# Optimization experiments

Measured on AMD Instinct MI355X. Metric: run time of the kernel, lower is better.

The kernel has to match this reference:

```python
import jax, jax.numpy as jnp
import numpy as np

N_NODES = 200000
N_EDGES = 3200000
N_FEAT = 128
N_GRAPHS = 1000
N_CLASSES = 10
K = 30          # sort-pool k
C_CAT = 97      # 32+32+32+1 concatenated channels


def _glorot(k, shape):
    fan = shape[0] + shape[-1]
    return jax.random.normal(k, shape, jnp.float32) * (2.0 / fan) ** 0.5


def setup_inputs() -> dict:
    key = jax.random.key(0)
    ks = jax.random.split(key, 20)
    x = jax.random.normal(ks[0], (N_NODES, N_FEAT), jnp.float32)
    edge_index = jax.random.randint(ks[1], (2, N_EDGES), 0, N_NODES, jnp.int32)
    batch = jnp.sort(jax.random.randint(ks[2], (N_NODES,), 0, N_GRAPHS, jnp.int32))
    params = dict(
        W1=_glorot(ks[3], (N_FEAT, 32)), b1=jnp.zeros((32,), jnp.float32),
        W2=_glorot(ks[4], (32, 32)),     b2=jnp.zeros((32,), jnp.float32),
        W3=_glorot(ks[5], (32, 32)),     b3=jnp.zeros((32,), jnp.float32),
        W4=_glorot(ks[6], (32, 1)),      b4=jnp.zeros((1,), jnp.float32),
        conv5_w=_glorot(ks[7], (16, 1, 97)),  conv5_b=jnp.zeros((16,), jnp.float32),
        conv6_w=_glorot(ks[8], (32, 16, 5)),  conv6_b=jnp.zeros((32,), jnp.float32),
        fc1_w=_glorot(ks[9], (352, 128)),     fc1_b=jnp.zeros((128,), jnp.float32),
        fc2_w=_glorot(ks[10], (128, N_CLASSES)), fc2_b=jnp.zeros((N_CLASSES,), jnp.float32),
    )
    return dict(x=x, edge_index=edge_index, batch=batch, **params)


def reference(x, edge_index, batch, W1, b1, W2, b2, W3, b3, W4, b4,
              conv5_w, conv5_b, conv6_w, conv6_b, fc1_w, fc1_b, fc2_w, fc2_b):
    N = x.shape[0]
    src, dst = edge_index[0], edge_index[1]
    emask = (src != dst).astype(x.dtype)            # remove_self_loops
    deg = jax.ops.segment_sum(emask, dst, num_segments=N) + 1.0  # +1 for added self-loop
    inv_sqrt = jax.lax.rsqrt(deg)
    coef = emask * inv_sqrt[src] * inv_sqrt[dst]    # D^-1/2 (A) D^-1/2 edge weight
    inv_deg = 1.0 / deg                             # self-loop weight

    def gcn(h, W, b):
        hw = h @ W
        agg = jax.ops.segment_sum(hw[src] * coef[:, None], dst, num_segments=N)
        return agg + hw * inv_deg[:, None] + b

    x1 = jnp.tanh(gcn(x, W1, b1))
    x2 = jnp.tanh(gcn(x1, W2, b2))
    x3 = jnp.tanh(gcn(x2, W3, b3))
    x4 = jnp.tanh(gcn(x3, W4, b4))
    xc = jnp.concatenate([x1, x2, x3, x4], axis=-1)  # [N, 97]

    # SortAggregation(k=30): per-graph descending sort by last channel, top-k, zero pad
    perm = jnp.lexsort((-xc[:, -1], batch))          # batch-major, last channel desc
    xs, bs = xc[perm], batch[perm]
    counts = jax.ops.segment_sum(jnp.ones_like(batch), batch, num_segments=N_GRAPHS)
    starts = jnp.cumsum(counts) - counts
    rank = jnp.arange(N, dtype=jnp.int32) - starts[bs]
    valid = rank < K
    pooled = jnp.zeros((N_GRAPHS, K, C_CAT), xc.dtype).at[
        bs, jnp.where(valid, rank, K - 1)].add(jnp.where(valid[:, None], xs, 0.0))

    z = pooled.reshape(N_GRAPHS, 1, K * C_CAT)       # [G, 1, 2910]
    dn = ('NCH', 'OIH', 'NCH')
    z = jax.lax.conv_general_dilated(z, conv5_w, (97,), 'VALID', dimension_numbers=dn)
    z = jax.nn.relu(z + conv5_b[None, :, None])      # [G, 16, 30]
    z = jax.lax.reduce_window(z, -jnp.inf, jax.lax.max, (1, 1, 2), (1, 1, 2), 'VALID')
    z = jax.lax.conv_general_dilated(z, conv6_w, (1,), 'VALID', dimension_numbers=dn)
    z = jax.nn.relu(z + conv6_b[None, :, None])      # [G, 32, 11]
    z = z.reshape(N_GRAPHS, -1)                      # [G, 352]
    h = jax.nn.relu(z @ fc1_w + fc1_b)               # dropout is identity in eval
    return jax.nn.log_softmax(h @ fc2_w + fc2_b, axis=-1)
```

## Files before the change

### kernel.cpp

```cpp
#include <hip/hip_runtime.h>
#include <math.h>

#define NN 200000
#define NE 3200000
#define NF 128
#define NG 1000
#define KSEL 30
#define CCAT 97
#define NPAD 200704
#define SCAN_BLKS 196

#define BWID 512
#define NB 391
#define BCAP 10240
#define P1_CHUNK 8192
#define P1_BLKS 391

__global__ void k_p1_partition(const int* __restrict__ ei, int* __restrict__ bcursor,
                               int* __restrict__ ebuf) {
    __shared__ int lhist[NB];
    __shared__ int lbase[NB];
    int tid = threadIdx.x;
    int base = blockIdx.x * P1_CHUNK;
    for (int b = tid; b < NB; b += 256) lhist[b] = 0;
    __syncthreads();
    for (int it = 0; it < P1_CHUNK / 256; it++) {
        int e = base + it * 256 + tid;
        if (e < NE) {
            int s = ei[e], d = ei[NE + e];
            if (s != d) atomicAdd(&lhist[d >> 9], 1);
        }
    }
    __syncthreads();
    for (int b = tid; b < NB; b += 256) {
        int cnt = lhist[b];
        lbase[b] = cnt ? atomicAdd(&bcursor[b], cnt) : 0;
        lhist[b] = 0;
    }
    __syncthreads();
    for (int it = 0; it < P1_CHUNK / 256; it++) {
        int e = base + it * 256 + tid;
        if (e < NE) {
            int s = ei[e], d = ei[NE + e];
            if (s != d) {
                int b = d >> 9;
                int r = atomicAdd(&lhist[b], 1);
                int pos = lbase[b] + r;
                if (pos >= BCAP) pos = BCAP - 1;
                ebuf[b * BCAP + pos] = s | ((d & 511) << 18);
            }
        }
    }
}

__global__ void k_p2_count(const int* __restrict__ bcursor, const int* __restrict__ ebuf,
                           int* __restrict__ rowcnt, float* __restrict__ inv_sqrt) {
    __shared__ int lcnt[BWID];
    int b = blockIdx.x;
    int tid = threadIdx.x;
    for (int i = tid; i < BWID; i += 256) lcnt[i] = 0;
    __syncthreads();
    int size = bcursor[b];
    if (size > BCAP) size = BCAP;
    const int* eb = ebuf + b * BCAP;
    for (int k = tid; k < size; k += 256) atomicAdd(&lcnt[eb[k] >> 18], 1);
    __syncthreads();
    int node0 = b * BWID;
    for (int i = tid; i < BWID; i += 256) {
        int node = node0 + i;
        if (node < NN) {
            int c = lcnt[i];
            rowcnt[node] = c;
            inv_sqrt[node] = rsqrtf((float)(c + 1));
        }
    }
}

__global__ void k_scanA(const int* __restrict__ in, int* __restrict__ out,
                        int* __restrict__ bsums) {
    __shared__ int s[1024];
    int tid = threadIdx.x;
    int gid = blockIdx.x * 1024 + tid;
    int v = in[gid];
    s[tid] = v;
    __syncthreads();
    for (int off = 1; off < 1024; off <<= 1) {
        int a = (tid >= off) ? s[tid - off] : 0;
        int cur = s[tid];
        __syncthreads();
        s[tid] = cur + a;
        __syncthreads();
    }
    out[gid] = s[tid] - v;
    if (tid == 1023) bsums[blockIdx.x] = s[tid];
}

__global__ void k_scanB(int* __restrict__ bsums) {
    __shared__ int s[256];
    int tid = threadIdx.x;
    int v = (tid < SCAN_BLKS) ? bsums[tid] : 0;
    s[tid] = v;
    __syncthreads();
    for (int off = 1; off < 256; off <<= 1) {
        int a = (tid >= off) ? s[tid - off] : 0;
        int cur = s[tid];
        __syncthreads();
        s[tid] = cur + a;
        __syncthreads();
    }
    if (tid < SCAN_BLKS) bsums[tid] = s[tid] - v;
}

__global__ void k_scanC(int* __restrict__ out, const int* __restrict__ bsums) {
    int gid = blockIdx.x * 1024 + threadIdx.x;
    out[gid] += bsums[blockIdx.x];
}

__global__ void k_p3_scatter(const int* __restrict__ bcursor, const int* __restrict__ ebuf,
                             const int* __restrict__ rowstart, int* __restrict__ esrc) {
    __shared__ int lcur[BWID];
    int b = blockIdx.x;
    int tid = threadIdx.x;
    int node0 = b * BWID;
    for (int i = tid; i < BWID; i += 256) lcur[i] = rowstart[node0 + i];
    __syncthreads();
    int size = bcursor[b];
    if (size > BCAP) size = BCAP;
    const int* eb = ebuf + b * BCAP;
    for (int k = tid; k < size; k += 256) {
        int v = eb[k];
        int local = v >> 18;
        int pos = atomicAdd(&lcur[local], 1);
        esrc[pos] = v & 0x3FFFF;
    }
}

template <int K>
__global__ void __launch_bounds__(256, 6) k_mm(const float* __restrict__ X,
                                               const float* __restrict__ W,
                                               const float* __restrict__ inv_sqrt,
                                               float* __restrict__ Y) {
    __shared__ float4 sW[K * 8];
    int tid = threadIdx.x;
    for (int i = tid; i < K * 8; i += 256) sW[i] = ((const float4*)W)[i];
    __syncthreads();
    int g = tid >> 3;
    int q = tid & 7;
    int r0 = blockIdx.x * 128 + g * 4;
    if (r0 >= NN) return;
    const float4* __restrict__ xp0 = (const float4*)(X + (size_t)(r0 + 0) * K);
    const float4* __restrict__ xp1 = (const float4*)(X + (size_t)(r0 + 1) * K);
    const float4* __restrict__ xp2 = (const float4*)(X + (size_t)(r0 + 2) * K);
    const float4* __restrict__ xp3 = (const float4*)(X + (size_t)(r0 + 3) * K);
    float4 a0 = make_float4(0.f, 0.f, 0.f, 0.f);
    float4 a1 = make_float4(0.f, 0.f, 0.f, 0.f);
    float4 a2 = make_float4(0.f, 0.f, 0.f, 0.f);
    float4 a3 = make_float4(0.f, 0.f, 0.f, 0.f);
#pragma unroll 2
    for (int k4 = 0; k4 < K / 4; k4++) {
        float4 x0 = xp0[k4];
        float4 x1 = xp1[k4];
        float4 x2 = xp2[k4];
        float4 x3 = xp3[k4];
        const float4* wk = &sW[k4 * 32 + q];
#pragma unroll
        for (int kk = 0; kk < 4; kk++) {
            float4 w = wk[kk * 8];
            float s0 = (kk == 0) ? x0.x : (kk == 1) ? x0.y : (kk == 2) ? x0.z : x0.w;
            float s1 = (kk == 0) ? x1.x : (kk == 1) ? x1.y : (kk == 2) ? x1.z : x1.w;
            float s2 = (kk == 0) ? x2.x : (kk == 1) ? x2.y : (kk == 2) ? x2.z : x2.w;
            float s3 = (kk == 0) ? x3.x : (kk == 1) ? x3.y : (kk == 2) ? x3.z : x3.w;
            a0.x = fmaf(s0, w.x, a0.x); a0.y = fmaf(s0, w.y, a0.y);
            a0.z = fmaf(s0, w.z, a0.z); a0.w = fmaf(s0, w.w, a0.w);
            a1.x = fmaf(s1, w.x, a1.x); a1.y = fmaf(s1, w.y, a1.y);
            a1.z = fmaf(s1, w.z, a1.z); a1.w = fmaf(s1, w.w, a1.w);
            a2.x = fmaf(s2, w.x, a2.x); a2.y = fmaf(s2, w.y, a2.y);
            a2.z = fmaf(s2, w.z, a2.z); a2.w = fmaf(s2, w.w, a2.w);
            a3.x = fmaf(s3, w.x, a3.x); a3.y = fmaf(s3, w.y, a3.y);
            a3.z = fmaf(s3, w.z, a3.z); a3.w = fmaf(s3, w.w, a3.w);
        }
    }
    float s0 = inv_sqrt[r0 + 0];
    float s1 = inv_sqrt[r0 + 1];
    float s2 = inv_sqrt[r0 + 2];
    float s3 = inv_sqrt[r0 + 3];
    a0.x *= s0; a0.y *= s0; a0.z *= s0; a0.w *= s0;
    a1.x *= s1; a1.y *= s1; a1.z *= s1; a1.w *= s1;
    a2.x *= s2; a2.y *= s2; a2.z *= s2; a2.w *= s2;
    a3.x *= s3; a3.y *= s3; a3.z *= s3; a3.w *= s3;
    ((float4*)(Y + (size_t)(r0 + 0) * 32))[q] = a0;
    ((float4*)(Y + (size_t)(r0 + 1) * 32))[q] = a1;
    ((float4*)(Y + (size_t)(r0 + 2) * 32))[q] = a2;
    ((float4*)(Y + (size_t)(r0 + 3) * 32))[q] = a3;
}

__global__ void k_aggr(const int* __restrict__ rowstart, const int* __restrict__ esrc,
                       const float* __restrict__ hws, const float* __restrict__ inv_sqrt,
                       const float* __restrict__ b, float* __restrict__ xout) {
    int t = blockIdx.x * 256 + threadIdx.x;
    int n = t >> 5, c = t & 31;
    if (n >= NN) return;
    int e0 = rowstart[n], e1 = rowstart[n + 1];
    float a[8];
    a[0] = hws[(size_t)n * 32 + c];
#pragma unroll
    for (int k = 1; k < 8; k++) a[k] = 0.0f;
    for (int e = e0; e < e1; e += 8) {
        int ss[8];
#pragma unroll
        for (int k = 0; k < 8; k++) ss[k] = esrc[(e + k < e1) ? e + k : e];
        float vv[8];
#pragma unroll
        for (int k = 0; k < 8; k++) vv[k] = hws[(size_t)ss[k] * 32 + c];
        a[0] += vv[0];
#pragma unroll
        for (int k = 1; k < 8; k++) a[k] += (e + k < e1) ? vv[k] : 0.0f;
    }
    float acc = ((a[0] + a[1]) + (a[2] + a[3])) + ((a[4] + a[5]) + (a[6] + a[7]));
    xout[t] = tanhf(fmaf(acc, inv_sqrt[n], b[c]));
}

__global__ void k_mm4(const float* __restrict__ x3, const float* __restrict__ W4,
                      const float* __restrict__ inv_sqrt, float* __restrict__ hws4) {
    int n = blockIdx.x * 256 + threadIdx.x;
    if (n >= NN) return;
    const float4* xr = (const float4*)(x3 + (size_t)n * 32);
    float acc = 0.0f;
#pragma unroll
    for (int q = 0; q < 8; q++) {
        float4 v = xr[q];
        acc = fmaf(v.x, W4[q * 4 + 0], acc);
        acc = fmaf(v.y, W4[q * 4 + 1], acc);
        acc = fmaf(v.z, W4[q * 4 + 2], acc);
        acc = fmaf(v.w, W4[q * 4 + 3], acc);
    }
    hws4[n] = acc * inv_sqrt[n];
}

__global__ void k_aggr1(const int* __restrict__ rowstart, const int* __restrict__ esrc,
                        const float* __restrict__ hws4, const float* __restrict__ inv_sqrt,
                        const float* __restrict__ b4, float* __restrict__ x4) {
    int n = blockIdx.x * 256 + threadIdx.x;
    if (n >= NN) return;
    int e0 = rowstart[n], e1 = rowstart[n + 1];
    float a[8];
    a[0] = hws4[n];
#pragma unroll
    for (int k = 1; k < 8; k++) a[k] = 0.0f;
    for (int e = e0; e < e1; e += 8) {
        int ss[8];
#pragma unroll
        for (int k = 0; k < 8; k++) ss[k] = esrc[(e + k < e1) ? e + k : e];
        float vv[8];
#pragma unroll
        for (int k = 0; k < 8; k++) vv[k] = hws4[ss[k]];
        a[0] += vv[0];
#pragma unroll
        for (int k = 1; k < 8; k++) a[k] += (e + k < e1) ? vv[k] : 0.0f;
    }
    float acc = ((a[0] + a[1]) + (a[2] + a[3])) + ((a[4] + a[5]) + (a[6] + a[7]));
    x4[n] = tanhf(fmaf(acc, inv_sqrt[n], b4[0]));
}

__global__ void k_gbounds(const int* __restrict__ batch, int* __restrict__ starts) {
    int n = blockIdx.x * 256 + threadIdx.x;
    if (n >= NN) return;
    int bn = batch[n];
    int bp = (n == 0) ? -1 : batch[n - 1];
    for (int g = bp + 1; g <= bn; g++) starts[g] = n;
    if (n == NN - 1)
        for (int g = bn + 1; g <= NG; g++) starts[g] = NN;
}

__global__ void k_sortpool(const int* __restrict__ starts,
                           const float* __restrict__ x1, const float* __restrict__ x2,
                           const float* __restrict__ x3, const float* __restrict__ x4,
                           float* __restrict__ pooled) {
    __shared__ float keys[1024];
    __shared__ int sel[KSEL];
    int g = blockIdx.x;
    int tid = threadIdx.x;
    int start = starts[g];
    int cnt = starts[g + 1] - start;
    if (cnt > 1024) cnt = 1024;
    for (int i = tid; i < cnt; i += 256) keys[i] = x4[start + i];
    __syncthreads();
    for (int i = tid; i < cnt; i += 256) {
        float ki = keys[i];
        int rank = 0;
        for (int j = 0; j < cnt; j++) {
            float kj = keys[j];
            rank += (kj > ki) || (kj == ki && j < i);
        }
        if (rank < KSEL) sel[rank] = start + i;
    }
    __syncthreads();
    int selcnt = cnt < KSEL ? cnt : KSEL;
    for (int t = tid; t < KSEL * CCAT; t += 256) {
        int r = t / CCAT, ch = t - r * CCAT;
        float v = 0.0f;
        if (r < selcnt) {
            int node = sel[r];
            if (ch < 32)      v = x1[(size_t)node * 32 + ch];
            else if (ch < 64) v = x2[(size_t)node * 32 + ch - 32];
            else if (ch < 96) v = x3[(size_t)node * 32 + ch - 64];
            else              v = x4[node];
        }
        pooled[g * (KSEL * CCAT) + t] = v;
    }
}

__global__ void k_head(const float* __restrict__ pooled,
                       const float* __restrict__ w5, const float* __restrict__ b5,
                       const float* __restrict__ w6, const float* __restrict__ b6,
                       const float* __restrict__ fw1, const float* __restrict__ fb1,
                       const float* __restrict__ fw2, const float* __restrict__ fb2,
                       float* __restrict__ out) {
    __shared__ float sP[KSEL * CCAT];
    __shared__ float s5[16 * 30];
    __shared__ float smp[16 * 15];
    __shared__ float sz[352];
    __shared__ float sh[128];
    __shared__ float sl[10];
    int g = blockIdx.x;
    int tid = threadIdx.x;
    for (int i = tid; i < KSEL * CCAT; i += 256) sP[i] = pooled[g * (KSEL * CCAT) + i];
    __syncthreads();
    for (int t = tid; t < 16 * 30; t += 256) {
        int c = t / 30, j = t - c * 30;
        float acc = b5[c];
        for (int i = 0; i < CCAT; i++) acc = fmaf(sP[j * CCAT + i], w5[c * CCAT + i], acc);
        s5[c * 30 + j] = fmaxf(acc, 0.0f);
    }
    __syncthreads();
    for (int t = tid; t < 16 * 15; t += 256) {
        int c = t / 15, j = t - c * 15;
        smp[t] = fmaxf(s5[c * 30 + 2 * j], s5[c * 30 + 2 * j + 1]);
    }
    __syncthreads();
    for (int t = tid; t < 32 * 11; t += 256) {
        int c = t / 11, j = t - c * 11;
        float acc = b6[c];
        for (int ci = 0; ci < 16; ci++) {
#pragma unroll
            for (int k = 0; k < 5; k++)
                acc = fmaf(smp[ci * 15 + j + k], w6[(c * 16 + ci) * 5 + k], acc);
        }
        sz[t] = fmaxf(acc, 0.0f);
    }
    __syncthreads();
    if (tid < 128) {
        float acc = fb1[tid];
        for (int i = 0; i < 352; i++) acc = fmaf(sz[i], fw1[i * 128 + tid], acc);
        sh[tid] = fmaxf(acc, 0.0f);
    }
    __syncthreads();
    if (tid < 10) {
        float acc = fb2[tid];
        for (int i = 0; i < 128; i++) acc = fmaf(sh[i], fw2[i * 10 + tid], acc);
        sl[tid] = acc;
    }
    __syncthreads();
    if (tid < 10) {
        float m = -1e30f;
        for (int i = 0; i < 10; i++) m = fmaxf(m, sl[i]);
        float ssum = 0.0f;
        for (int i = 0; i < 10; i++) ssum += expf(sl[i] - m);
        out[g * 10 + tid] = sl[tid] - m - logf(ssum);
    }
}

extern "C" void kernel_launch(void* const* d_in, const int* in_sizes, int n_in,
                              void* d_out, int out_size, void* d_ws, size_t ws_size,
                              hipStream_t stream) {
    const float* x   = (const float*)d_in[0];
    const int*   ei  = (const int*)d_in[1];
    const int*   bat = (const int*)d_in[2];
    const float* W1  = (const float*)d_in[3];
    const float* b1  = (const float*)d_in[4];
    const float* W2  = (const float*)d_in[5];
    const float* b2  = (const float*)d_in[6];
    const float* W3  = (const float*)d_in[7];
    const float* b3  = (const float*)d_in[8];
    const float* W4  = (const float*)d_in[9];
    const float* b4  = (const float*)d_in[10];
    const float* w5  = (const float*)d_in[11];
    const float* b5  = (const float*)d_in[12];
    const float* w6  = (const float*)d_in[13];
    const float* b6  = (const float*)d_in[14];
    const float* fw1 = (const float*)d_in[15];
    const float* fb1 = (const float*)d_in[16];
    const float* fw2 = (const float*)d_in[17];
    const float* fb2 = (const float*)d_in[18];
    float* out = (float*)d_out;

    float* ws = (float*)d_ws;
    float* inv_sqrt = ws;
    float* hws      = inv_sqrt + NN;
    float* x1       = hws + (size_t)NN * 32;
    float* x2       = x1 + (size_t)NN * 32;
    float* x3       = x2 + (size_t)NN * 32;
    float* x4       = x3 + (size_t)NN * 32;
    float* pooled   = x4 + NN;
    int* rowcnt     = (int*)(pooled + NG * KSEL * CCAT);
    int* rowstart   = rowcnt + NPAD;
    int* esrc       = rowstart + NPAD;
    int* bcursor    = esrc + NE;
    int* bsums      = bcursor + 512;
    int* gstarts    = bsums + 256;
    int* ebuf       = (int*)x3;

    const int TB = 256;
    int gN  = (NN + TB - 1) / TB;
    int gNC = (NN * 32 + TB - 1) / TB;
    int gMM = (NN + 127) / 128;

    hipMemsetAsync(bcursor, 0, 512 * sizeof(int), stream);
    hipMemsetAsync(rowcnt, 0, NPAD * sizeof(int), stream);
    k_p1_partition<<<P1_BLKS, TB, 0, stream>>>(ei, bcursor, ebuf);
    k_p2_count<<<NB, TB, 0, stream>>>(bcursor, ebuf, rowcnt, inv_sqrt);
    k_scanA<<<SCAN_BLKS, 1024, 0, stream>>>(rowcnt, rowstart, bsums);
    k_scanB<<<1, 256, 0, stream>>>(bsums);
    k_scanC<<<SCAN_BLKS, 1024, 0, stream>>>(rowstart, bsums);
    k_p3_scatter<<<NB, TB, 0, stream>>>(bcursor, ebuf, rowstart, esrc);

    k_gbounds<<<gN, TB, 0, stream>>>(bat, gstarts);

    k_mm<128><<<gMM, TB, 0, stream>>>(x, W1, inv_sqrt, hws);
    k_aggr<<<gNC, TB, 0, stream>>>(rowstart, esrc, hws, inv_sqrt, b1, x1);
    k_mm<32><<<gMM, TB, 0, stream>>>(x1, W2, inv_sqrt, hws);
    k_aggr<<<gNC, TB, 0, stream>>>(rowstart, esrc, hws, inv_sqrt, b2, x2);
    k_mm<32><<<gMM, TB, 0, stream>>>(x2, W3, inv_sqrt, hws);
    k_aggr<<<gNC, TB, 0, stream>>>(rowstart, esrc, hws, inv_sqrt, b3, x3);
    k_mm4<<<gN, TB, 0, stream>>>(x3, W4, inv_sqrt, hws);
    k_aggr1<<<gN, TB, 0, stream>>>(rowstart, esrc, hws, inv_sqrt, b4, x4);

    k_sortpool<<<NG, TB, 0, stream>>>(gstarts, x1, x2, x3, x4, pooled);
    k_head<<<NG, TB, 0, stream>>>(pooled, w5, b5, w6, b6, fw1, fb1, fw2, fb2, out);
}
```

Measured before the change: 597.1 us.

## Vectorize CSR aggregation with float4 gathers over four edges per node

```diff
diff --git a/kernel.cpp b/kernel.cpp
--- a/kernel.cpp
+++ b/kernel.cpp
@@ -136,7 +136,7 @@
 }
 
 template <int K>
-__global__ void __launch_bounds__(256, 6) k_mm(const float* __restrict__ X,
+__global__ void __launch_bounds__(256, 4) k_mm(const float* __restrict__ X,
                                                const float* __restrict__ W,
                                                const float* __restrict__ inv_sqrt,
                                                float* __restrict__ Y) {
@@ -156,7 +156,7 @@
     float4 a1 = make_float4(0.f, 0.f, 0.f, 0.f);
     float4 a2 = make_float4(0.f, 0.f, 0.f, 0.f);
     float4 a3 = make_float4(0.f, 0.f, 0.f, 0.f);
-#pragma unroll 2
+#pragma unroll 4
     for (int k4 = 0; k4 < K / 4; k4++) {
         float4 x0 = xp0[k4];
         float4 x1 = xp1[k4];
@@ -198,26 +198,48 @@
                        const float* __restrict__ hws, const float* __restrict__ inv_sqrt,
                        const float* __restrict__ b, float* __restrict__ xout) {
     int t = blockIdx.x * 256 + threadIdx.x;
-    int n = t >> 5, c = t & 31;
+    int n = t >> 5;
     if (n >= NN) return;
+    int l = threadIdx.x & 31;
+    int slot = l >> 3;
+    int q = l & 7;
+    const float4* __restrict__ hp = (const float4*)hws;
     int e0 = rowstart[n], e1 = rowstart[n + 1];
-    float a[8];
-    a[0] = hws[(size_t)n * 32 + c];
-#pragma unroll
-    for (int k = 1; k < 8; k++) a[k] = 0.0f;
-    for (int e = e0; e < e1; e += 8) {
-        int ss[8];
-#pragma unroll
-        for (int k = 0; k < 8; k++) ss[k] = esrc[(e + k < e1) ? e + k : e];
-        float vv[8];
-#pragma unroll
-        for (int k = 0; k < 8; k++) vv[k] = hws[(size_t)ss[k] * 32 + c];
-        a[0] += vv[0];
-#pragma unroll
-        for (int k = 1; k < 8; k++) a[k] += (e + k < e1) ? vv[k] : 0.0f;
-    }
-    float acc = ((a[0] + a[1]) + (a[2] + a[3])) + ((a[4] + a[5]) + (a[6] + a[7]));
-    xout[t] = tanhf(fmaf(acc, inv_sqrt[n], b[c]));
+    int cnt = e1 - e0;
+    float4 acc = make_float4(0.f, 0.f, 0.f, 0.f);
+    int nfull = cnt >> 2;
+    int e = e0;
+#pragma unroll 2
+    for (int it = 0; it < nfull; it++, e += 4) {
+        int idx = esrc[e + slot];
+        float4 v = hp[idx * 8 + q];
+        acc.x += v.x; acc.y += v.y; acc.z += v.z; acc.w += v.w;
+    }
+    int rem = cnt & 3;
+    if (slot < rem) {
+        int idx = esrc[e + slot];
+        float4 v = hp[idx * 8 + q];
+        acc.x += v.x; acc.y += v.y; acc.z += v.z; acc.w += v.w;
+    }
+    acc.x += __shfl_xor(acc.x, 8);
+    acc.y += __shfl_xor(acc.y, 8);
+    acc.z += __shfl_xor(acc.z, 8);
+    acc.w += __shfl_xor(acc.w, 8);
+    acc.x += __shfl_xor(acc.x, 16);
+    acc.y += __shfl_xor(acc.y, 16);
+    acc.z += __shfl_xor(acc.z, 16);
+    acc.w += __shfl_xor(acc.w, 16);
+    if (slot == 0) {
+        float4 self = hp[n * 8 + q];
+        float4 bq = ((const float4*)b)[q];
+        float is = inv_sqrt[n];
+        float4 r;
+        r.x = tanhf(fmaf(acc.x + self.x, is, bq.x));
+        r.y = tanhf(fmaf(acc.y + self.y, is, bq.y));
+        r.z = tanhf(fmaf(acc.z + self.z, is, bq.z));
+        r.w = tanhf(fmaf(acc.w + self.w, is, bq.w));
+        ((float4*)(xout + (size_t)n * 32))[q] = r;
+    }
 }
 
 __global__ void k_mm4(const float* __restrict__ x3, const float* __restrict__ W4,
```

Result: slower. 619.0 us (+3.7%).
